# Performance work log

Measured on AMD Instinct MI355X. Metric: run time of the kernel, lower is better.

The kernel has to match this reference:

```python
import jax, jax.numpy as jnp
import numpy as np

B = 1024
D = 512
M = 65536          # num_memory
C = 4096           # num pseudo-label clusters (= labels.max()+1, fixed for jit)
TEMP = 0.05
EPS = 1e-6


def setup_inputs() -> dict:
    key = jax.random.key(0)
    k1, k2, k3, k4 = jax.random.split(key, 4)
    inputs = jax.random.normal(k1, (B, D), dtype=jnp.float32)
    indexes = jax.random.randint(k2, (B,), 0, M, dtype=jnp.int64)
    feats = jax.random.normal(k3, (M, D), dtype=jnp.float32)
    # memory bank stores L2-normalized features (see _update_feature)
    features = feats / jnp.linalg.norm(feats, axis=1, keepdims=True)
    labels = jax.random.randint(k4, (M,), 0, C, dtype=jnp.int64)
    return {"inputs": inputs, "indexes": indexes, "features": features, "labels": labels}


def reference(inputs, indexes, features, labels):
    # F.normalize(inputs, p=2, dim=1)
    x = inputs / jnp.linalg.norm(inputs, axis=1, keepdims=True)
    # HM.forward: inputs @ features.T, then / temp  -> sim over memory slots [B, M]
    sim = (x @ features.T) / TEMP
    # index_add over labels: per-cluster sum of sim columns  -> [C, B]
    sim_c = jax.ops.segment_sum(sim.T, labels, num_segments=C)
    nums = jax.ops.segment_sum(jnp.ones((M,), dtype=sim.dtype), labels, num_segments=C)  # [C]
    cluster_mask = (nums > 0).astype(sim.dtype)                     # [C]
    # mean within cluster; empty clusters divide by 1
    avg = sim_c / jnp.where(nums > 0, nums, 1.0)[:, None]           # [C, B]
    # masked_softmax over clusters, per sample
    vec = avg.T                                                     # [B, C]
    masked_exps = jnp.exp(vec) * cluster_mask[None, :]
    probs = masked_exps / (jnp.sum(masked_exps, axis=1, keepdims=True) + EPS)
    # F.nll_loss(log(probs + eps), targets) with targets = labels[indexes]
    targets = labels[indexes]                                       # [B]
    logp = jnp.log(probs + EPS)
    loss = -jnp.mean(logp[jnp.arange(B), targets])
    return loss
```

## Files before the change

### kernel.cpp

```cpp
#include <hip/hip_runtime.h>
#include <hip/hip_bf16.h>

#define NB 1024
#define ND 512
#define NM 65536
#define NC 4096

static constexpr float TEMP = 0.05f;
static constexpr float EPSF = 1e-6f;

typedef __attribute__((ext_vector_type(8))) short short8v;
typedef __attribute__((ext_vector_type(16))) float f32x16;

static __device__ __forceinline__ short f2bf(float f) {
    __hip_bfloat16 h = __float2bfloat16(f);
    return *reinterpret_cast<short*>(&h);
}

__global__ __launch_bounds__(256) void k_zero_tgt(const int* __restrict__ indexes,
                                                  const int* __restrict__ labels,
                                                  int* __restrict__ counts,
                                                  float* __restrict__ denom,
                                                  int* __restrict__ tgt) {
    int i = blockIdx.x * 256 + threadIdx.x;
    if (i < NC) counts[i] = 0;
    if (i < NB) {
        denom[i] = 0.f;
        tgt[i] = labels[indexes[i]];
    }
}

__global__ __launch_bounds__(128) void k_normalize(const float* __restrict__ in,
                                                   short* __restrict__ xnb) {
    int b = blockIdx.x;
    const float4* row = reinterpret_cast<const float4*>(in + (size_t)b * ND);
    float4 v = row[threadIdx.x];
    float ss = v.x * v.x + v.y * v.y + v.z * v.z + v.w * v.w;
#pragma unroll
    for (int o = 32; o > 0; o >>= 1) ss += __shfl_down(ss, o);
    __shared__ float sw[2];
    int lane = threadIdx.x & 63, w = threadIdx.x >> 6;
    if (lane == 0) sw[w] = ss;
    __syncthreads();
    float inv = 1.0f / sqrtf(sw[0] + sw[1]);
    short4 o;
    o.x = f2bf(v.x * inv); o.y = f2bf(v.y * inv);
    o.z = f2bf(v.z * inv); o.w = f2bf(v.w * inv);
    reinterpret_cast<short4*>(xnb + (size_t)b * ND)[threadIdx.x] = o;
}

__global__ __launch_bounds__(256) void k_count(const int* __restrict__ labels,
                                               int* __restrict__ counts) {
    int m = blockIdx.x * 256 + threadIdx.x;
    if (m < NM) atomicAdd(&counts[labels[m]], 1);
}

__global__ __launch_bounds__(256) void k_scan(const int* __restrict__ counts,
                                              int* __restrict__ starts,
                                              int* __restrict__ cursor) {
    __shared__ int part[256];
    int t = threadIdx.x;
    int local[16];
    int base = t * 16;
    int s = 0;
#pragma unroll
    for (int i = 0; i < 16; ++i) { local[i] = counts[base + i]; s += local[i]; }
    part[t] = s;
    __syncthreads();
    for (int off = 1; off < 256; off <<= 1) {
        int v = (t >= off) ? part[t - off] : 0;
        __syncthreads();
        part[t] += v;
        __syncthreads();
    }
    int excl = (t == 0) ? 0 : part[t - 1];
#pragma unroll
    for (int i = 0; i < 16; ++i) {
        starts[base + i] = excl;
        cursor[base + i] = excl;
        excl += local[i];
    }
}

__global__ __launch_bounds__(256) void k_scatter(const int* __restrict__ labels,
                                                 int* __restrict__ cursor,
                                                 int* __restrict__ idx) {
    int m = blockIdx.x * 256 + threadIdx.x;
    int c = labels[m];
    int pos = atomicAdd(&cursor[c], 1);
    idx[pos] = m;
}

__global__ __launch_bounds__(128) void k_gather(const float* __restrict__ feats,
                                                const int* __restrict__ idx,
                                                const int* __restrict__ starts,
                                                const int* __restrict__ counts,
                                                short* __restrict__ Gb) {
    int c = blockIdx.x;
    int t = threadIdx.x;
    int s0 = starts[c];
    int n = counts[c];
    const float4* F = reinterpret_cast<const float4*>(feats);
    float4 a0 = {0.f, 0.f, 0.f, 0.f};
    float4 a1 = {0.f, 0.f, 0.f, 0.f};
    int j = 0;
    for (; j + 1 < n; j += 2) {
        int m0 = idx[s0 + j];
        int m1 = idx[s0 + j + 1];
        float4 v0 = F[(size_t)m0 * 128 + t];
        float4 v1 = F[(size_t)m1 * 128 + t];
        a0.x += v0.x; a0.y += v0.y; a0.z += v0.z; a0.w += v0.w;
        a1.x += v1.x; a1.y += v1.y; a1.z += v1.z; a1.w += v1.w;
    }
    if (j < n) {
        int m0 = idx[s0 + j];
        float4 v0 = F[(size_t)m0 * 128 + t];
        a0.x += v0.x; a0.y += v0.y; a0.z += v0.z; a0.w += v0.w;
    }
    short4 o;
    o.x = f2bf(a0.x + a1.x); o.y = f2bf(a0.y + a1.y);
    o.z = f2bf(a0.z + a1.z); o.w = f2bf(a0.w + a1.w);
    reinterpret_cast<short4*>(Gb + (size_t)c * ND)[t] = o;
}

__global__ __launch_bounds__(256) void k_gemm_mfma(const short* __restrict__ A,
                                                   const short* __restrict__ Bm,
                                                   const int* __restrict__ counts,
                                                   const int* __restrict__ tgt,
                                                   float* __restrict__ denom,
                                                   float* __restrict__ numer) {
    const int tid = threadIdx.x;
    const int w = tid >> 6;
    const int lane = tid & 63;
    const int ln = lane & 31;
    const int kg = lane >> 5;
    const int row0 = blockIdx.y * 128 + (w >> 1) * 64;
    const int col0 = blockIdx.x * 128 + (w & 1) * 64;

    f32x16 acc00 = {}, acc01 = {}, acc10 = {}, acc11 = {};
    const short* pa0 = A + (size_t)(row0 + ln) * ND + kg * 8;
    const short* pa1 = pa0 + 32 * ND;
    const short* pb0 = Bm + (size_t)(col0 + ln) * ND + kg * 8;
    const short* pb1 = pb0 + 32 * ND;
#pragma unroll 4
    for (int k0 = 0; k0 < ND; k0 += 16) {
        short8v a0 = *reinterpret_cast<const short8v*>(pa0 + k0);
        short8v a1 = *reinterpret_cast<const short8v*>(pa1 + k0);
        short8v b0 = *reinterpret_cast<const short8v*>(pb0 + k0);
        short8v b1 = *reinterpret_cast<const short8v*>(pb1 + k0);
        acc00 = __builtin_amdgcn_mfma_f32_32x32x16_bf16(a0, b0, acc00, 0, 0, 0);
        acc01 = __builtin_amdgcn_mfma_f32_32x32x16_bf16(a0, b1, acc01, 0, 0, 0);
        acc10 = __builtin_amdgcn_mfma_f32_32x32x16_bf16(a1, b0, acc10, 0, 0, 0);
        acc11 = __builtin_amdgcn_mfma_f32_32x32x16_bf16(a1, b1, acc11, 0, 0, 0);
    }
    int colA = col0 + ln;
    int colB = colA + 32;
    int nA = counts[colA], nB = counts[colB];
    float invA = 1.0f / (TEMP * (float)(nA > 0 ? nA : 1));
    float invB = 1.0f / (TEMP * (float)(nB > 0 ? nB : 1));
    float mA = (nA > 0) ? 1.f : 0.f;
    float mB = (nB > 0) ? 1.f : 0.f;
    int rbase = row0 + 4 * kg;
#pragma unroll
    for (int r = 0; r < 16; ++r) {
        int row = rbase + (r & 3) + 8 * (r >> 2);
        int rowH = row + 32;
        float v00 = acc00[r] * invA, v01 = acc01[r] * invB;
        float v10 = acc10[r] * invA, v11 = acc11[r] * invB;
        int t0 = tgt[row], t1 = tgt[rowH];
        if (t0 == colA) numer[row] = v00;
        if (t0 == colB) numer[row] = v01;
        if (t1 == colA) numer[rowH] = v10;
        if (t1 == colB) numer[rowH] = v11;
        float s0 = mA * __expf(v00) + mB * __expf(v01);
        float s1 = mA * __expf(v10) + mB * __expf(v11);
#pragma unroll
        for (int m = 1; m < 32; m <<= 1) {
            s0 += __shfl_xor(s0, m);
            s1 += __shfl_xor(s1, m);
        }
        if (ln == 0) {
            atomicAdd(&denom[row], s0);
            atomicAdd(&denom[rowH], s1);
        }
    }
}

__global__ __launch_bounds__(256) void k_final(const float* __restrict__ numer,
                                               const float* __restrict__ denom,
                                               float* __restrict__ out) {
    float s = 0.f;
    for (int i = threadIdx.x; i < NB; i += 256) {
        float p = __expf(numer[i]) / (denom[i] + EPSF);
        s += -logf(p + EPSF);
    }
#pragma unroll
    for (int o = 32; o > 0; o >>= 1) s += __shfl_down(s, o);
    __shared__ float sw[4];
    int lane = threadIdx.x & 63, w = threadIdx.x >> 6;
    if (lane == 0) sw[w] = s;
    __syncthreads();
    if (threadIdx.x == 0) out[0] = (sw[0] + sw[1] + sw[2] + sw[3]) / (float)NB;
}

extern "C" void kernel_launch(void* const* d_in, const int* in_sizes, int n_in,
                              void* d_out, int out_size, void* d_ws, size_t ws_size,
                              hipStream_t stream) {
    const float* inputs   = (const float*)d_in[0];
    const int*   indexes  = (const int*)d_in[1];
    const float* features = (const float*)d_in[2];
    const int*   labels   = (const int*)d_in[3];
    float* out = (float*)d_out;

    short* Gb     = (short*)d_ws;
    short* xnb    = Gb + (size_t)NC * ND;
    float* denom  = (float*)(xnb + (size_t)NB * ND);
    float* numer  = denom + NB;
    int*   tgt    = (int*)(numer + NB);
    int*   counts = tgt + NB;
    int*   starts = counts + NC;
    int*   cursor = starts + NC;
    int*   idx    = cursor + NC;

    k_zero_tgt<<<16, 256, 0, stream>>>(indexes, labels, counts, denom, tgt);
    k_normalize<<<NB, 128, 0, stream>>>(inputs, xnb);
    k_count<<<NM / 256, 256, 0, stream>>>(labels, counts);
    k_scan<<<1, 256, 0, stream>>>(counts, starts, cursor);
    k_scatter<<<NM / 256, 256, 0, stream>>>(labels, cursor, idx);
    k_gather<<<NC, 128, 0, stream>>>(features, idx, starts, counts, Gb);
    dim3 g(NC / 128, NB / 128);
    k_gemm_mfma<<<g, 256, 0, stream>>>(xnb, Gb, counts, tgt, denom, numer);
    k_final<<<1, 256, 0, stream>>>(numer, denom, out);
}
```

Before: 86.49 us.

## Fuse launches: merge init into normalize, histogram+scan via last-block, final into GEMM

Cuts the launch count from eight to five. Init work moves into the normalize kernel, and the global-atomic count plus single-block scan become a 16-block shared-memory histogram whose last block reduces the partial histograms and runs the scan. The final loss reduction now runs in the last-finishing GEMM block, found through an atomic ticket counter. The gather loop is unrolled to four independent loads, which adds memory-level parallelism. The ticket counters rely on threadfence ordering, and the last-block reductions run serially on one block.

```diff
diff --git a/kernel.cpp b/kernel.cpp
--- a/kernel.cpp
+++ b/kernel.cpp
@@ -17,21 +17,13 @@
     return *reinterpret_cast<short*>(&h);
 }
 
-__global__ __launch_bounds__(256) void k_zero_tgt(const int* __restrict__ indexes,
-                                                  const int* __restrict__ labels,
-                                                  int* __restrict__ counts,
-                                                  float* __restrict__ denom,
-                                                  int* __restrict__ tgt) {
-    int i = blockIdx.x * 256 + threadIdx.x;
-    if (i < NC) counts[i] = 0;
-    if (i < NB) {
-        denom[i] = 0.f;
-        tgt[i] = labels[indexes[i]];
-    }
-}
-
-__global__ __launch_bounds__(128) void k_normalize(const float* __restrict__ in,
-                                                   short* __restrict__ xnb) {
+__global__ __launch_bounds__(128) void k_norm_init(const float* __restrict__ in,
+                                                   const int* __restrict__ indexes,
+                                                   const int* __restrict__ labels,
+                                                   short* __restrict__ xnb,
+                                                   int* __restrict__ tgt,
+                                                   float* __restrict__ denom,
+                                                   int* __restrict__ flags) {
     int b = blockIdx.x;
     const float4* row = reinterpret_cast<const float4*>(in + (size_t)b * ND);
     float4 v = row[threadIdx.x];
@@ -47,45 +39,69 @@
     o.x = f2bf(v.x * inv); o.y = f2bf(v.y * inv);
     o.z = f2bf(v.z * inv); o.w = f2bf(v.w * inv);
     reinterpret_cast<short4*>(xnb + (size_t)b * ND)[threadIdx.x] = o;
-}
-
-__global__ __launch_bounds__(256) void k_count(const int* __restrict__ labels,
-                                               int* __restrict__ counts) {
-    int m = blockIdx.x * 256 + threadIdx.x;
-    if (m < NM) atomicAdd(&counts[labels[m]], 1);
-}
-
-__global__ __launch_bounds__(256) void k_scan(const int* __restrict__ counts,
-                                              int* __restrict__ starts,
-                                              int* __restrict__ cursor) {
-    __shared__ int part[256];
-    int t = threadIdx.x;
-    int local[16];
-    int base = t * 16;
+    if (threadIdx.x == 0) {
+        tgt[b] = labels[indexes[b]];
+        denom[b] = 0.f;
+        if (b < 2) flags[b] = 0;
+    }
+}
+
+__global__ __launch_bounds__(1024) void k_hist_scan(const int* __restrict__ labels,
+                                                    int* __restrict__ phist,
+                                                    int* __restrict__ counts,
+                                                    int* __restrict__ starts,
+                                                    int* __restrict__ cursor,
+                                                    int* __restrict__ flags) {
+    __shared__ int hist[NC];
+    __shared__ int lastflag;
+    int t = threadIdx.x, blk = blockIdx.x;
+    for (int c = t; c < NC; c += 1024) hist[c] = 0;
+    __syncthreads();
+    const int* lab = labels + blk * 4096;
+    for (int i = t; i < 4096; i += 1024) atomicAdd(&hist[lab[i]], 1);
+    __syncthreads();
+    for (int c = t; c < NC; c += 1024) phist[blk * NC + c] = hist[c];
+    __threadfence();
+    __syncthreads();
+    if (t == 0) lastflag = (atomicAdd(&flags[0], 1) == 15) ? 1 : 0;
+    __syncthreads();
+    if (!lastflag) return;
+    __threadfence();
+    int base = t * 4;
+    int local[4];
     int s = 0;
 #pragma unroll
-    for (int i = 0; i < 16; ++i) { local[i] = counts[base + i]; s += local[i]; }
-    part[t] = s;
-    __syncthreads();
-    for (int off = 1; off < 256; off <<= 1) {
-        int v = (t >= off) ? part[t - off] : 0;
+    for (int i = 0; i < 4; ++i) {
+        int c = base + i;
+        int v = 0;
+#pragma unroll
+        for (int k = 0; k < 16; ++k) v += phist[k * NC + c];
+        local[i] = v;
+        s += v;
+        counts[c] = v;
+    }
+    __syncthreads();
+    hist[t] = s;
+    __syncthreads();
+    for (int off = 1; off < 1024; off <<= 1) {
+        int v = (t >= off) ? hist[t - off] : 0;
         __syncthreads();
-        part[t] += v;
+        hist[t] += v;
         __syncthreads();
     }
-    int excl = (t == 0) ? 0 : part[t - 1];
-#pragma unroll
-    for (int i = 0; i < 16; ++i) {
+    int excl = (t == 0) ? 0 : hist[t - 1];
+#pragma unroll
+    for (int i = 0; i < 4; ++i) {
         starts[base + i] = excl;
         cursor[base + i] = excl;
         excl += local[i];
     }
 }
 
-__global__ __launch_bounds__(256) void k_scatter(const int* __restrict__ labels,
-                                                 int* __restrict__ cursor,
-                                                 int* __restrict__ idx) {
-    int m = blockIdx.x * 256 + threadIdx.x;
+__global__ __launch_bounds__(1024) void k_scatter(const int* __restrict__ labels,
+                                                  int* __restrict__ cursor,
+                                                  int* __restrict__ idx) {
+    int m = blockIdx.x * 1024 + threadIdx.x;
     int c = labels[m];
     int pos = atomicAdd(&cursor[c], 1);
     idx[pos] = m;
@@ -101,34 +117,42 @@
     int s0 = starts[c];
     int n = counts[c];
     const float4* F = reinterpret_cast<const float4*>(feats);
-    float4 a0 = {0.f, 0.f, 0.f, 0.f};
-    float4 a1 = {0.f, 0.f, 0.f, 0.f};
+    float4 a0 = {0.f, 0.f, 0.f, 0.f}, a1 = {0.f, 0.f, 0.f, 0.f};
+    float4 a2 = {0.f, 0.f, 0.f, 0.f}, a3 = {0.f, 0.f, 0.f, 0.f};
     int j = 0;
-    for (; j + 1 < n; j += 2) {
-        int m0 = idx[s0 + j];
-        int m1 = idx[s0 + j + 1];
+    for (; j + 3 < n; j += 4) {
+        int m0 = idx[s0 + j], m1 = idx[s0 + j + 1];
+        int m2 = idx[s0 + j + 2], m3 = idx[s0 + j + 3];
         float4 v0 = F[(size_t)m0 * 128 + t];
         float4 v1 = F[(size_t)m1 * 128 + t];
+        float4 v2 = F[(size_t)m2 * 128 + t];
+        float4 v3 = F[(size_t)m3 * 128 + t];
         a0.x += v0.x; a0.y += v0.y; a0.z += v0.z; a0.w += v0.w;
         a1.x += v1.x; a1.y += v1.y; a1.z += v1.z; a1.w += v1.w;
-    }
-    if (j < n) {
+        a2.x += v2.x; a2.y += v2.y; a2.z += v2.z; a2.w += v2.w;
+        a3.x += v3.x; a3.y += v3.y; a3.z += v3.z; a3.w += v3.w;
+    }
+    for (; j < n; ++j) {
         int m0 = idx[s0 + j];
         float4 v0 = F[(size_t)m0 * 128 + t];
         a0.x += v0.x; a0.y += v0.y; a0.z += v0.z; a0.w += v0.w;
     }
     short4 o;
-    o.x = f2bf(a0.x + a1.x); o.y = f2bf(a0.y + a1.y);
-    o.z = f2bf(a0.z + a1.z); o.w = f2bf(a0.w + a1.w);
+    o.x = f2bf(a0.x + a1.x + a2.x + a3.x);
+    o.y = f2bf(a0.y + a1.y + a2.y + a3.y);
+    o.z = f2bf(a0.z + a1.z + a2.z + a3.z);
+    o.w = f2bf(a0.w + a1.w + a2.w + a3.w);
     reinterpret_cast<short4*>(Gb + (size_t)c * ND)[t] = o;
 }
 
-__global__ __launch_bounds__(256) void k_gemm_mfma(const short* __restrict__ A,
-                                                   const short* __restrict__ Bm,
-                                                   const int* __restrict__ counts,
-                                                   const int* __restrict__ tgt,
-                                                   float* __restrict__ denom,
-                                                   float* __restrict__ numer) {
+__global__ __launch_bounds__(256) void k_gemm_final(const short* __restrict__ A,
+                                                    const short* __restrict__ Bm,
+                                                    const int* __restrict__ counts,
+                                                    const int* __restrict__ tgt,
+                                                    float* __restrict__ denom,
+                                                    float* __restrict__ numer,
+                                                    int* __restrict__ flags,
+                                                    float* __restrict__ out) {
     const int tid = threadIdx.x;
     const int w = tid >> 6;
     const int lane = tid & 63;
@@ -184,23 +208,24 @@
             atomicAdd(&denom[rowH], s1);
         }
     }
-}
-
-__global__ __launch_bounds__(256) void k_final(const float* __restrict__ numer,
-                                               const float* __restrict__ denom,
-                                               float* __restrict__ out) {
+    __threadfence();
+    __syncthreads();
+    __shared__ int lastf;
+    if (tid == 0) lastf = (atomicAdd(&flags[1], 1) == 255) ? 1 : 0;
+    __syncthreads();
+    if (!lastf) return;
+    __threadfence();
     float s = 0.f;
-    for (int i = threadIdx.x; i < NB; i += 256) {
+    for (int i = tid; i < NB; i += 256) {
         float p = __expf(numer[i]) / (denom[i] + EPSF);
         s += -logf(p + EPSF);
     }
 #pragma unroll
     for (int o = 32; o > 0; o >>= 1) s += __shfl_down(s, o);
     __shared__ float sw[4];
-    int lane = threadIdx.x & 63, w = threadIdx.x >> 6;
     if (lane == 0) sw[w] = s;
     __syncthreads();
-    if (threadIdx.x == 0) out[0] = (sw[0] + sw[1] + sw[2] + sw[3]) / (float)NB;
+    if (tid == 0) out[0] = (sw[0] + sw[1] + sw[2] + sw[3]) / (float)NB;
 }
 
 extern "C" void kernel_launch(void* const* d_in, const int* in_sizes, int n_in,
@@ -217,18 +242,17 @@
     float* denom  = (float*)(xnb + (size_t)NB * ND);
     float* numer  = denom + NB;
     int*   tgt    = (int*)(numer + NB);
-    int*   counts = tgt + NB;
+    int*   flags  = tgt + NB;
+    int*   counts = flags + 2;
     int*   starts = counts + NC;
     int*   cursor = starts + NC;
-    int*   idx    = cursor + NC;
-
-    k_zero_tgt<<<16, 256, 0, stream>>>(indexes, labels, counts, denom, tgt);
-    k_normalize<<<NB, 128, 0, stream>>>(inputs, xnb);
-    k_count<<<NM / 256, 256, 0, stream>>>(labels, counts);
-    k_scan<<<1, 256, 0, stream>>>(counts, starts, cursor);
-    k_scatter<<<NM / 256, 256, 0, stream>>>(labels, cursor, idx);
+    int*   phist  = cursor + NC;
+    int*   idx    = phist + 16 * NC;
+
+    k_norm_init<<<NB, 128, 0, stream>>>(inputs, indexes, labels, xnb, tgt, denom, flags);
+    k_hist_scan<<<16, 1024, 0, stream>>>(labels, phist, counts, starts, cursor, flags);
+    k_scatter<<<NM / 1024, 1024, 0, stream>>>(labels, cursor, idx);
     k_gather<<<NC, 128, 0, stream>>>(features, idx, starts, counts, Gb);
     dim3 g(NC / 128, NB / 128);
-    k_gemm_mfma<<<g, 256, 0, stream>>>(xnb, Gb, counts, tgt, denom, numer);
-    k_final<<<1, 256, 0, stream>>>(numer, denom, out);
-}
+    k_gemm_final<<<g, 256, 0, stream>>>(xnb, Gb, counts, tgt, denom, numer, flags, out);
+}
```

Result: slower. 105.6 us (+22.1%).

## Fuse init into normalize, merge count and scan via last-block flag, unroll gather

Applied to the files above, without the earlier changes.

Folds the zero/target-init kernel into the normalize kernel, and merges the label histogram and prefix scan into one kernel where the last block to finish (detected with an atomic counter and threadfences) performs the scan. This cuts two kernel launches and their serialization gaps. The gather loop is also unrolled to four independent accumulators to keep more loads in flight. The cost is a grid-wide atomic completion counter, fence overhead, and a slightly different summation order.

```diff
diff --git a/kernel.cpp b/kernel.cpp
--- a/kernel.cpp
+++ b/kernel.cpp
@@ -17,49 +17,54 @@
     return *reinterpret_cast<short*>(&h);
 }
 
-__global__ __launch_bounds__(256) void k_zero_tgt(const int* __restrict__ indexes,
-                                                  const int* __restrict__ labels,
-                                                  int* __restrict__ counts,
-                                                  float* __restrict__ denom,
-                                                  int* __restrict__ tgt) {
-    int i = blockIdx.x * 256 + threadIdx.x;
-    if (i < NC) counts[i] = 0;
-    if (i < NB) {
-        denom[i] = 0.f;
-        tgt[i] = labels[indexes[i]];
-    }
-}
-
-__global__ __launch_bounds__(128) void k_normalize(const float* __restrict__ in,
-                                                   short* __restrict__ xnb) {
+__global__ __launch_bounds__(128) void k_norm_init(const float* __restrict__ in,
+                                                   const int* __restrict__ indexes,
+                                                   const int* __restrict__ labels,
+                                                   short* __restrict__ xnb,
+                                                   int* __restrict__ tgt,
+                                                   float* __restrict__ denom,
+                                                   int* __restrict__ counts,
+                                                   int* __restrict__ flags) {
     int b = blockIdx.x;
+    int t = threadIdx.x;
     const float4* row = reinterpret_cast<const float4*>(in + (size_t)b * ND);
-    float4 v = row[threadIdx.x];
+    float4 v = row[t];
     float ss = v.x * v.x + v.y * v.y + v.z * v.z + v.w * v.w;
 #pragma unroll
     for (int o = 32; o > 0; o >>= 1) ss += __shfl_down(ss, o);
     __shared__ float sw[2];
-    int lane = threadIdx.x & 63, w = threadIdx.x >> 6;
+    int lane = t & 63, w = t >> 6;
     if (lane == 0) sw[w] = ss;
     __syncthreads();
     float inv = 1.0f / sqrtf(sw[0] + sw[1]);
     short4 o;
     o.x = f2bf(v.x * inv); o.y = f2bf(v.y * inv);
     o.z = f2bf(v.z * inv); o.w = f2bf(v.w * inv);
-    reinterpret_cast<short4*>(xnb + (size_t)b * ND)[threadIdx.x] = o;
-}
-
-__global__ __launch_bounds__(256) void k_count(const int* __restrict__ labels,
-                                               int* __restrict__ counts) {
-    int m = blockIdx.x * 256 + threadIdx.x;
-    if (m < NM) atomicAdd(&counts[labels[m]], 1);
-}
-
-__global__ __launch_bounds__(256) void k_scan(const int* __restrict__ counts,
-                                              int* __restrict__ starts,
-                                              int* __restrict__ cursor) {
+    reinterpret_cast<short4*>(xnb + (size_t)b * ND)[t] = o;
+    if (b < 32) counts[b * 128 + t] = 0;
+    if (t == 0) {
+        tgt[b] = labels[indexes[b]];
+        denom[b] = 0.f;
+        if (b == 0) flags[0] = 0;
+    }
+}
+
+__global__ __launch_bounds__(256) void k_count_scan(const int* __restrict__ labels,
+                                                    int* __restrict__ counts,
+                                                    int* __restrict__ starts,
+                                                    int* __restrict__ cursor,
+                                                    int* __restrict__ flags) {
+    int t = threadIdx.x;
+    int m = blockIdx.x * 256 + t;
+    atomicAdd(&counts[labels[m]], 1);
+    __threadfence();
+    __syncthreads();
+    __shared__ int lastf;
+    if (t == 0) lastf = (atomicAdd(&flags[0], 1) == 255) ? 1 : 0;
+    __syncthreads();
+    if (!lastf) return;
+    __threadfence();
     __shared__ int part[256];
-    int t = threadIdx.x;
     int local[16];
     int base = t * 16;
     int s = 0;
@@ -101,25 +106,31 @@
     int s0 = starts[c];
     int n = counts[c];
     const float4* F = reinterpret_cast<const float4*>(feats);
-    float4 a0 = {0.f, 0.f, 0.f, 0.f};
-    float4 a1 = {0.f, 0.f, 0.f, 0.f};
+    float4 a0 = {0.f, 0.f, 0.f, 0.f}, a1 = {0.f, 0.f, 0.f, 0.f};
+    float4 a2 = {0.f, 0.f, 0.f, 0.f}, a3 = {0.f, 0.f, 0.f, 0.f};
     int j = 0;
-    for (; j + 1 < n; j += 2) {
-        int m0 = idx[s0 + j];
-        int m1 = idx[s0 + j + 1];
+    for (; j + 3 < n; j += 4) {
+        int m0 = idx[s0 + j], m1 = idx[s0 + j + 1];
+        int m2 = idx[s0 + j + 2], m3 = idx[s0 + j + 3];
         float4 v0 = F[(size_t)m0 * 128 + t];
         float4 v1 = F[(size_t)m1 * 128 + t];
+        float4 v2 = F[(size_t)m2 * 128 + t];
+        float4 v3 = F[(size_t)m3 * 128 + t];
         a0.x += v0.x; a0.y += v0.y; a0.z += v0.z; a0.w += v0.w;
         a1.x += v1.x; a1.y += v1.y; a1.z += v1.z; a1.w += v1.w;
-    }
-    if (j < n) {
+        a2.x += v2.x; a2.y += v2.y; a2.z += v2.z; a2.w += v2.w;
+        a3.x += v3.x; a3.y += v3.y; a3.z += v3.z; a3.w += v3.w;
+    }
+    for (; j < n; ++j) {
         int m0 = idx[s0 + j];
         float4 v0 = F[(size_t)m0 * 128 + t];
         a0.x += v0.x; a0.y += v0.y; a0.z += v0.z; a0.w += v0.w;
     }
     short4 o;
-    o.x = f2bf(a0.x + a1.x); o.y = f2bf(a0.y + a1.y);
-    o.z = f2bf(a0.z + a1.z); o.w = f2bf(a0.w + a1.w);
+    o.x = f2bf(a0.x + a1.x + a2.x + a3.x);
+    o.y = f2bf(a0.y + a1.y + a2.y + a3.y);
+    o.z = f2bf(a0.z + a1.z + a2.z + a3.z);
+    o.w = f2bf(a0.w + a1.w + a2.w + a3.w);
     reinterpret_cast<short4*>(Gb + (size_t)c * ND)[t] = o;
 }
 
@@ -217,15 +228,14 @@
     float* denom  = (float*)(xnb + (size_t)NB * ND);
     float* numer  = denom + NB;
     int*   tgt    = (int*)(numer + NB);
-    int*   counts = tgt + NB;
+    int*   flags  = tgt + NB;
+    int*   counts = flags + 4;
     int*   starts = counts + NC;
     int*   cursor = starts + NC;
     int*   idx    = cursor + NC;
 
-    k_zero_tgt<<<16, 256, 0, stream>>>(indexes, labels, counts, denom, tgt);
-    k_normalize<<<NB, 128, 0, stream>>>(inputs, xnb);
-    k_count<<<NM / 256, 256, 0, stream>>>(labels, counts);
-    k_scan<<<1, 256, 0, stream>>>(counts, starts, cursor);
+    k_norm_init<<<NB, 128, 0, stream>>>(inputs, indexes, labels, xnb, tgt, denom, counts, flags);
+    k_count_scan<<<NM / 256, 256, 0, stream>>>(labels, counts, starts, cursor, flags);
     k_scatter<<<NM / 256, 256, 0, stream>>>(labels, cursor, idx);
     k_gather<<<NC, 128, 0, stream>>>(features, idx, starts, counts, Gb);
     dim3 g(NC / 128, NB / 128);
```

New measurement: 93.39 us. 8.0% more time.
